# Kernel tuning notes

Measured on AMD Instinct MI355X. Metric: run time of the kernel, lower is better.

Reference implementation:

```python
import jax, jax.numpy as jnp
import numpy as np

NUM_HEADS = 12
TEMPORAL_RES = 8


def _ln(x, g, b, eps=1e-5):
    mu = jnp.mean(x, axis=-1, keepdims=True)
    var = jnp.mean((x - mu) ** 2, axis=-1, keepdims=True)
    return (x - mu) * jax.lax.rsqrt(var + eps) * g + b


def setup_inputs() -> dict:
    key = jax.random.key(0)
    ks = jax.random.split(key, 8)
    s = 0.02
    d = 768
    inp = {
        'box_tensors': jax.random.uniform(ks[0], (16, 16, 10, 4), dtype=jnp.float32),
        'box_categories': jax.random.normal(ks[1], (16, 10, d), dtype=jnp.float32) * s,
        'w1': jax.random.normal(ks[2], (4, d // 2), dtype=jnp.float32) * s,
        'w2': jax.random.normal(ks[3], (d // 2, d), dtype=jnp.float32) * s,
        'ln1_g': jnp.ones((d,), jnp.float32),
        'ln1_b': jnp.zeros((d,), jnp.float32),
        'wqkv': jax.random.normal(ks[4], (d, 3 * d), dtype=jnp.float32) * s,
        'wo': jax.random.normal(ks[5], (d, d), dtype=jnp.float32) * s,
        'bo': jnp.zeros((d,), jnp.float32),
        'ln2_g': jnp.ones((d,), jnp.float32),
        'ln2_b': jnp.zeros((d,), jnp.float32),
        'wfc1': jax.random.normal(ks[6], (d, 4 * d), dtype=jnp.float32) * s,
        'bfc1': jnp.zeros((4 * d,), jnp.float32),
        'wfc2': jax.random.normal(ks[7], (4 * d, d), dtype=jnp.float32) * s,
        'bfc2': jnp.zeros((d,), jnp.float32),
        'H': 14,
        'W': 14,
    }
    return inp


def _forward(box_tensors, box_categories, w1, w2, ln1_g, ln1_b, wqkv, wo, bo,
             ln2_g, ln2_b, wfc1, bfc1, wfc2, bfc2, H, W):
    B, T, O, _ = box_tensors.shape
    d = box_categories.shape[-1]
    # coord -> feature MLP (no biases), then pos-emb add
    h = jax.nn.relu(box_tensors @ w1)
    x = jax.nn.relu(h @ w2)                      # [B,T,O,d]
    x = x + box_categories[None]                 # broadcast over batch
    L = T * O
    x = x.reshape(B, L, d)
    # --- self-attention block (pre-LN ViT style) ---
    hn = _ln(x, ln1_g, ln1_b)
    qkv = (hn @ wqkv).reshape(B, L, 3, NUM_HEADS, d // NUM_HEADS)
    q, k, v = qkv[:, :, 0], qkv[:, :, 1], qkv[:, :, 2]   # [B,L,h,dh]
    scale = 1.0 / jnp.sqrt(jnp.asarray(d // NUM_HEADS, x.dtype))
    att = jnp.einsum('bqhd,bkhd->bhqk', q, k) * scale
    att = jax.nn.softmax(att, axis=-1)
    o = jnp.einsum('bhqk,bkhd->bqhd', att, v).reshape(B, L, d)
    x = x + (o @ wo + bo)
    hn = _ln(x, ln2_g, ln2_b)
    x = x + (jax.nn.gelu(hn @ wfc1 + bfc1, approximate=False) @ wfc2 + bfc2)
    feats = x.reshape(B, T, O, d)
    # --- box2spatial layout scatter: sum each object's feature into grid cells inside its box ---
    x1 = jnp.minimum(box_tensors[..., 0], box_tensors[..., 2])
    x2 = jnp.maximum(box_tensors[..., 0], box_tensors[..., 2])
    y1 = jnp.minimum(box_tensors[..., 1], box_tensors[..., 3])
    y2 = jnp.maximum(box_tensors[..., 1], box_tensors[..., 3])
    cy = (jnp.arange(H, dtype=x.dtype) + 0.5) / H    # [H]
    cx = (jnp.arange(W, dtype=x.dtype) + 0.5) / W    # [W]
    in_y = (cy[None, None, None, :] >= y1[..., None]) & (cy[None, None, None, :] <= y2[..., None])  # [B,T,O,H]
    in_x = (cx[None, None, None, :] >= x1[..., None]) & (cx[None, None, None, :] <= x2[..., None])  # [B,T,O,W]
    mask = (in_y[..., :, None] & in_x[..., None, :]).astype(x.dtype)  # [B,T,O,H,W]
    grid = jnp.einsum('btohw,btod->bthwd', mask, feats)               # [B,T,H,W,d]
    # temporal avg pooling to TEMPORAL_RES frames
    Tr = T // TEMPORAL_RES
    if Tr > 1:
        grid = grid.reshape(B, T // Tr, Tr, H, W, d).mean(axis=2)
    return grid.reshape(B, -1, d)                 # [B, T'*H*W, d]


def reference(box_tensors, box_categories, w1, w2, ln1_g, ln1_b, wqkv, wo, bo,
              ln2_g, ln2_b, wfc1, bfc1, wfc2, bfc2, H, W):
    return _forward(box_tensors, box_categories, w1, w2, ln1_g, ln1_b, wqkv, wo, bo,
                    ln2_g, ln2_b, wfc1, bfc1, wfc2, bfc2, H, W)
```

## Files before the change

kernel.cpp:

```cpp
#include <hip/hip_runtime.h>
#include <hip/hip_bf16.h>
#include <math.h>


#define BATCH 16
#define TT    16
#define OO    10
#define LL    160
#define BL    2560
#define DD    768
#define NH    12
#define DH    64
#define GH    14
#define GW    14
#define TGRP  8

typedef unsigned short ushort_t;
typedef __attribute__((ext_vector_type(8))) __bf16 bf16x8;
typedef __attribute__((ext_vector_type(4))) float f32x4;

__device__ __forceinline__ ushort_t f2bf(float f) {
    unsigned int u = __float_as_uint(f);
    u += 0x7fffu + ((u >> 16) & 1u);
    return (ushort_t)(u >> 16);
}

__device__ __forceinline__ int swz_xcd(int bid, int nwg) {
    return (bid & 7) * (nwg >> 3) + (bid >> 3);
}

__global__ __launch_bounds__(256)
void prep_all(const float* __restrict__ wqkv, const float* __restrict__ wo,
              const float* __restrict__ wfc1, const float* __restrict__ wfc2,
              const float* __restrict__ w2, const float* __restrict__ box,
              const float* __restrict__ w1,
              ushort_t* __restrict__ wqkvT, ushort_t* __restrict__ woT,
              ushort_t* __restrict__ wfc1T, ushort_t* __restrict__ wfc2T,
              ushort_t* __restrict__ w2T, ushort_t* __restrict__ h)
{
    __shared__ float s[32][33];
    int t = blockIdx.x;
    const float* W; ushort_t* Wt; int K, N, nx;
    if (t < 1728)      {            W = wqkv; Wt = wqkvT; K = 768;  N = 2304; nx = 72; }
    else if (t < 2304) { t -= 1728; W = wo;   Wt = woT;   K = 768;  N = 768;  nx = 24; }
    else if (t < 4608) { t -= 2304; W = wfc1; Wt = wfc1T; K = 768;  N = 3072; nx = 96; }
    else if (t < 6912) { t -= 4608; W = wfc2; Wt = wfc2T; K = 3072; N = 768;  nx = 24; }
    else if (t < 7200) { t -= 6912; W = w2;   Wt = w2T;   K = 384;  N = 768;  nx = 24; }
    else {
        const int i2 = (t - 7200) * 256 + threadIdx.x;
        const int r = i2 / 384, j = i2 - r * 384;
        const float* bx = box + (size_t)r * 4;
        float v = bx[0] * w1[j] + bx[1] * w1[384 + j] +
                  bx[2] * w1[768 + j] + bx[3] * w1[1152 + j];
        h[i2] = f2bf(fmaxf(v, 0.f));
        return;
    }
    const int n0 = (t % nx) * 32, k0 = (t / nx) * 32;
    const int tx = threadIdx.x & 31, ty = threadIdx.x >> 5;
#pragma unroll
    for (int r = 0; r < 4; ++r)
        s[ty + r * 8][tx] = W[(size_t)(k0 + ty + r * 8) * N + n0 + tx];
    __syncthreads();
#pragma unroll
    for (int r = 0; r < 4; ++r)
        Wt[(size_t)(n0 + ty + r * 8) * K + k0 + tx] = f2bf(s[tx][ty + r * 8]);
}

__global__ __launch_bounds__(256)
void ln_kernel(const float* __restrict__ in, const float* __restrict__ g,
               const float* __restrict__ bvec, ushort_t* __restrict__ out)
{
    const int r = blockIdx.x;
    const int tid = threadIdx.x;
    const float* row = in + (size_t)r * DD;
    float v0 = row[tid], v1 = row[tid + 256], v2 = row[tid + 512];
    float s  = v0 + v1 + v2;
    float s2 = v0 * v0 + v1 * v1 + v2 * v2;
#pragma unroll
    for (int off = 32; off > 0; off >>= 1) {
        s  += __shfl_down(s, off);
        s2 += __shfl_down(s2, off);
    }
    __shared__ float red[8];
    int wave = tid >> 6, lane = tid & 63;
    if (lane == 0) { red[wave] = s; red[wave + 4] = s2; }
    __syncthreads();
    s  = red[0] + red[1] + red[2] + red[3];
    s2 = red[4] + red[5] + red[6] + red[7];
    float mu  = s * (1.f / DD);
    float var = s2 * (1.f / DD) - mu * mu;
    float inv = rsqrtf(var + 1e-5f);
    ushort_t* op = out + (size_t)r * DD;
    op[tid]       = f2bf((v0 - mu) * inv * g[tid]       + bvec[tid]);
    op[tid + 256] = f2bf((v1 - mu) * inv * g[tid + 256] + bvec[tid + 256]);
    op[tid + 512] = f2bf((v2 - mu) * inv * g[tid + 512] + bvec[tid + 512]);
}

template <int MI, int NJ, int MODE, int SPLIT>
__global__ __launch_bounds__(64)
void gemm_rf2(const ushort_t* __restrict__ A, int lda,
              const ushort_t* __restrict__ Bt, int ldb,
              const float* __restrict__ bias, const float* __restrict__ cat,
              float* __restrict__ Cf, ushort_t* __restrict__ Cb,
              int ldc, int K)
{
    const int lane = threadIdx.x;
    const int l16 = lane & 15, quad = lane >> 4;

    const int nwg = gridDim.x * gridDim.y * gridDim.z;
    const int bid = blockIdx.x + gridDim.x * (blockIdx.y + gridDim.y * blockIdx.z);
    const int w   = swz_xcd(bid, nwg);
    const int bx  = w % gridDim.x;
    const int byz = w / gridDim.x;
    const int by  = byz % gridDim.y;
    const int bz  = byz / gridDim.y;

    const int row0 = by * (MI * 16), col0 = bx * (NJ * 16);
    const int Kper = K / SPLIT;
    const int k0   = bz * Kper;

    const ushort_t* ap = A  + (size_t)(row0 + l16) * lda + k0 + quad * 8;
    const ushort_t* bp = Bt + (size_t)(col0 + l16) * ldb + k0 + quad * 8;

    f32x4 acc[MI][NJ];
#pragma unroll
    for (int i = 0; i < MI; ++i)
#pragma unroll
        for (int j = 0; j < NJ; ++j) {
            acc[i][j][0] = 0.f; acc[i][j][1] = 0.f;
            acc[i][j][2] = 0.f; acc[i][j][3] = 0.f;
        }

#define LOADF2(aa, bb, kk)                                                       \
    _Pragma("unroll")                                                            \
    for (int i = 0; i < MI; ++i)                                                 \
        aa[i] = *reinterpret_cast<const bf16x8*>(ap + (size_t)(i * 16) * lda + (kk)); \
    _Pragma("unroll")                                                            \
    for (int j = 0; j < NJ; ++j)                                                 \
        bb[j] = *reinterpret_cast<const bf16x8*>(bp + (size_t)(j * 16) * ldb + (kk));
#define MFMA2(aa, bb)                                                            \
    _Pragma("unroll")                                                            \
    for (int i = 0; i < MI; ++i)                                                 \
        _Pragma("unroll")                                                        \
        for (int j = 0; j < NJ; ++j)                                             \
            acc[i][j] = __builtin_amdgcn_mfma_f32_16x16x32_bf16(aa[i], bb[j], acc[i][j], 0, 0, 0);

    bf16x8 a0[MI], b0[NJ], a1[MI], b1[NJ];
    LOADF2(a0, b0, 0)
    int kt = 0;
    for (; kt + 64 < Kper; kt += 64) {
        LOADF2(a1, b1, kt + 32)
        MFMA2(a0, b0)
        LOADF2(a0, b0, kt + 64)
        MFMA2(a1, b1)
    }
    LOADF2(a1, b1, kt + 32)
    MFMA2(a0, b0)
    MFMA2(a1, b1)
#undef LOADF2
#undef MFMA2

    const int q4 = quad * 4;
#pragma unroll
    for (int i = 0; i < MI; ++i)
#pragma unroll
        for (int j = 0; j < NJ; ++j) {
            const int gcol = col0 + j * 16 + l16;
            const float bj = (MODE == 1 || MODE == 2) ? bias[gcol] : 0.f;
#pragma unroll
            for (int r = 0; r < 4; ++r) {
                const int grow = row0 + i * 16 + q4 + r;
                const size_t idx = (size_t)grow * ldc + gcol;
                const float v = acc[i][j][r];
                if (MODE == 1) {
                    Cf[idx] += v + bj;
                } else if (MODE == 2) {
                    const float u = v + bj;
                    Cb[idx] = f2bf(0.5f * u * (1.f + erff(u * 0.70710678118654752f)));
                } else if (MODE == 3) {
                    Cb[idx] = f2bf(v);
                } else {
                    Cf[idx] = fmaxf(v, 0.f) + cat[(size_t)(grow % LL) * DD + gcol];
                }
            }
        }
}

#define GLL(gp, lp) __builtin_amdgcn_global_load_lds(                       \
    (const __attribute__((address_space(1))) void*)(gp),                     \
    (__attribute__((address_space(3))) void*)(lp), 16, 0, 0)

template <int MODE, int SPLIT>
__global__ __launch_bounds__(256)
void gemm_lds(const ushort_t* __restrict__ A, int lda,
              const ushort_t* __restrict__ Bt, int ldb,
              const float* __restrict__ bias,
              float* __restrict__ Cf, ushort_t* __restrict__ Cb,
              int ldc, int K)
{
    __shared__ ushort_t As[2][8192];
    __shared__ ushort_t Bs[2][8192];

    const int t    = threadIdx.x;
    const int wv   = t >> 6;
    const int lane = t & 63;
    const int l16  = lane & 15, quad = lane >> 4;
    const int wr   = (wv >> 1) * 64;
    const int wc   = (wv & 1) * 64;

    const int nwg = gridDim.x * gridDim.y * gridDim.z;
    const int bid = blockIdx.x + gridDim.x * (blockIdx.y + gridDim.y * blockIdx.z);
    const int w   = swz_xcd(bid, nwg);
    const int bx  = w % gridDim.x;
    const int byz = w / gridDim.x;
    const int by  = byz % gridDim.y;
    const int bz  = byz / gridDim.y;

    const int row0 = by * 128, col0 = bx * 128;
    const int Kper = K / SPLIT;
    const int k0   = bz * Kper;
    const int steps = Kper / 64;

    const ushort_t* Ag = A  + (size_t)(row0 + (t & 127)) * lda + k0 + ((t >> 7) * 8);
    const ushort_t* Bg = Bt + (size_t)(col0 + (t & 127)) * ldb + k0 + ((t >> 7) * 8);

#define STAGE(c, kk) do {                                                    \
        _Pragma("unroll")                                                    \
        for (int ii = 0; ii < 4; ++ii) {                                     \
            GLL(Ag + (kk) + ii * 16, &As[c][ii * 2048 + wv * 512]);          \
            GLL(Bg + (kk) + ii * 16, &Bs[c][ii * 2048 + wv * 512]);          \
        }                                                                    \
    } while (0)

    f32x4 acc[4][4];
#pragma unroll
    for (int i = 0; i < 4; ++i)
#pragma unroll
        for (int j = 0; j < 4; ++j) {
            acc[i][j][0] = 0.f; acc[i][j][1] = 0.f;
            acc[i][j][2] = 0.f; acc[i][j][3] = 0.f;
        }

    STAGE(0, 0);
    __syncthreads();
    int cur = 0;
    for (int s = 0; s < steps; ++s) {
        if (s + 1 < steps) STAGE(cur ^ 1, (s + 1) * 64);
#pragma unroll
        for (int ks = 0; ks < 2; ++ks) {
            bf16x8 af[4], bfr[4];
#pragma unroll
            for (int i = 0; i < 4; ++i)
                af[i] = *reinterpret_cast<const bf16x8*>(
                    &As[cur][((ks * 4 + quad) * 128 + wr + i * 16 + l16) * 8]);
#pragma unroll
            for (int j = 0; j < 4; ++j)
                bfr[j] = *reinterpret_cast<const bf16x8*>(
                    &Bs[cur][((ks * 4 + quad) * 128 + wc + j * 16 + l16) * 8]);
#pragma unroll
            for (int i = 0; i < 4; ++i)
#pragma unroll
                for (int j = 0; j < 4; ++j)
                    acc[i][j] = __builtin_amdgcn_mfma_f32_16x16x32_bf16(
                        af[i], bfr[j], acc[i][j], 0, 0, 0);
        }
        __syncthreads();
        cur ^= 1;
    }
#undef STAGE

    const int q4 = quad * 4;
    const int r0w = row0 + wr, c0w = col0 + wc;
#pragma unroll
    for (int i = 0; i < 4; ++i)
#pragma unroll
        for (int j = 0; j < 4; ++j) {
            const int gcol = c0w + j * 16 + l16;
            const float bj = (MODE == 1 || MODE == 2)
                               ? ((SPLIT == 1 || bz == 0) ? bias[gcol] : 0.f)
                               : 0.f;
#pragma unroll
            for (int r = 0; r < 4; ++r) {
                const int grow = r0w + i * 16 + q4 + r;
                const size_t idx = (size_t)grow * ldc + gcol;
                const float v = acc[i][j][r];
                if (MODE == 1) {
                    if (SPLIT > 1) atomicAdd(&Cf[idx], v + bj);
                    else           Cf[idx] += v + bj;
                } else if (MODE == 2) {
                    const float u = v + bj;
                    Cb[idx] = f2bf(0.5f * u * (1.f + erff(u * 0.70710678118654752f)));
                } else {
                    Cb[idx] = f2bf(v);
                }
            }
        }
}

#define KS_STRIDE 72
#define VT_STRIDE 168
__global__ __launch_bounds__(320)
void attention_mfma(ushort_t* __restrict__ qkv)
{
    __shared__ ushort_t Ks[160 * KS_STRIDE];
    __shared__ ushort_t Vt[64 * VT_STRIDE];
    __shared__ ushort_t Pb[5][16 * VT_STRIDE];

    const int half = blockIdx.x;
    const int b  = blockIdx.y / NH;
    const int hh = blockIdx.y % NH;
    ushort_t* basew = qkv + (size_t)b * LL * (3 * DD) + hh * DH;
    const ushort_t* base = basew;
    const int tid  = threadIdx.x;
    const int wave = tid >> 6, lane = tid & 63;
    const int l16 = lane & 15, quad = lane >> 4;

#pragma unroll
    for (int it = 0; it < 4; ++it) {
        int idx = tid + it * 320;
        int l = idx >> 3, c8 = (idx & 7) * 8;
        uint4 kv = *(const uint4*)(base + (size_t)l * (3 * DD) + DD + c8);
        *(uint4*)&Ks[l * KS_STRIDE + c8] = kv;
        uint4 vv = *(const uint4*)(base + (size_t)l * (3 * DD) + 2 * DD + c8);
        ushort_t e[8];
        *(uint4*)e = vv;
#pragma unroll
        for (int i = 0; i < 8; ++i)
            Vt[(c8 + i) * VT_STRIDE + l] = e[i];
    }

    const int q0 = half * 80 + wave * 16;
    bf16x8 qf[2];
#pragma unroll
    for (int k = 0; k < 2; ++k)
        qf[k] = *reinterpret_cast<const bf16x8*>(
            base + (size_t)(q0 + l16) * (3 * DD) + k * 32 + quad * 8);

    __syncthreads();

    f32x4 S[10];
#pragma unroll
    for (int nt = 0; nt < 10; ++nt) {
        f32x4 z = {0.f, 0.f, 0.f, 0.f};
        const ushort_t* kb = &Ks[(nt * 16 + l16) * KS_STRIDE + quad * 8];
        bf16x8 kf0 = *reinterpret_cast<const bf16x8*>(kb);
        bf16x8 kf1 = *reinterpret_cast<const bf16x8*>(kb + 32);
        f32x4 a0 = __builtin_amdgcn_mfma_f32_16x16x32_bf16(qf[0], kf0, z, 0, 0, 0);
        S[nt]    = __builtin_amdgcn_mfma_f32_16x16x32_bf16(qf[1], kf1, a0, 0, 0, 0);
    }

    {
        float mrow[4] = {-1e30f, -1e30f, -1e30f, -1e30f};
#pragma unroll
        for (int nt = 0; nt < 10; ++nt)
#pragma unroll
            for (int r = 0; r < 4; ++r) {
                S[nt][r] *= 0.125f;
                mrow[r] = fmaxf(mrow[r], S[nt][r]);
            }
#pragma unroll
        for (int r = 0; r < 4; ++r) {
            mrow[r] = fmaxf(mrow[r], __shfl_xor(mrow[r], 1));
            mrow[r] = fmaxf(mrow[r], __shfl_xor(mrow[r], 2));
            mrow[r] = fmaxf(mrow[r], __shfl_xor(mrow[r], 4));
            mrow[r] = fmaxf(mrow[r], __shfl_xor(mrow[r], 8));
        }
        float lsum[4] = {0.f, 0.f, 0.f, 0.f};
#pragma unroll
        for (int nt = 0; nt < 10; ++nt)
#pragma unroll
            for (int r = 0; r < 4; ++r) {
                float e = __expf(S[nt][r] - mrow[r]);
                S[nt][r] = e;
                lsum[r] += e;
            }
#pragma unroll
        for (int r = 0; r < 4; ++r) {
            lsum[r] += __shfl_xor(lsum[r], 1);
            lsum[r] += __shfl_xor(lsum[r], 2);
            lsum[r] += __shfl_xor(lsum[r], 4);
            lsum[r] += __shfl_xor(lsum[r], 8);
            lsum[r] = 1.f / lsum[r];
        }
#pragma unroll
        for (int nt = 0; nt < 10; ++nt)
#pragma unroll
            for (int r = 0; r < 4; ++r)
                Pb[wave][(quad * 4 + r) * VT_STRIDE + nt * 16 + l16] =
                    f2bf(S[nt][r] * lsum[r]);
    }
    asm volatile("s_waitcnt lgkmcnt(0)" ::: "memory");

#pragma unroll
    for (int dt = 0; dt < 4; ++dt) {
        f32x4 o0 = {0.f, 0.f, 0.f, 0.f};
#pragma unroll
        for (int ks = 0; ks < 5; ++ks) {
            bf16x8 vf = *reinterpret_cast<const bf16x8*>(
                &Vt[(dt * 16 + l16) * VT_STRIDE + ks * 32 + quad * 8]);
            bf16x8 p0 = *reinterpret_cast<const bf16x8*>(
                &Pb[wave][(l16) * VT_STRIDE + ks * 32 + quad * 8]);
            o0 = __builtin_amdgcn_mfma_f32_16x16x32_bf16(vf, p0, o0, 0, 0, 0);
        }
        ushort_t pk[4];
#pragma unroll
        for (int r = 0; r < 4; ++r) pk[r] = f2bf(o0[r]);
        ushort_t* dst = basew + (size_t)(q0 + l16) * (3 * DD) + dt * 16 + quad * 4;
        *(uint2*)dst = *(const uint2*)pk;
    }
}

__global__ __launch_bounds__(256)
void mask_grid(const float* __restrict__ box, const float* __restrict__ feats,
               float* __restrict__ out)
{
    const int bx2 = blockIdx.x;
    const int g = blockIdx.y;
    const int b = blockIdx.z;
    const int hh = bx2 >> 1, w0 = (bx2 & 1) * 7;
    const float cy = (hh + 0.5f) / (float)GH;
    const int tid = threadIdx.x;

    __shared__ float x1s[20], x2s[20];
    if (tid < 20) {
        int t = g * 2 + tid / OO, o = tid % OO;
        const float* bp = box + (size_t)((b * TT + t) * OO + o) * 4;
        float x1 = fminf(bp[0], bp[2]), x2 = fmaxf(bp[0], bp[2]);
        float y1 = fminf(bp[1], bp[3]), y2 = fmaxf(bp[1], bp[3]);
        bool yok = (cy >= y1) && (cy <= y2);
        x1s[tid] = yok ? x1 : 2.f;
        x2s[tid] = yok ? x2 : -2.f;
    }

    float fr[20][3];
#pragma unroll
    for (int p = 0; p < 20; ++p) {
        int r = (b * TT + g * 2 + p / OO) * OO + (p % OO);
        const float* f = feats + (size_t)r * DD;
        fr[p][0] = f[tid];
        fr[p][1] = f[tid + 256];
        fr[p][2] = f[tid + 512];
    }
    __syncthreads();

    float* obase = out + ((size_t)(b * TGRP + g) * (GH * GW) + hh * GW + w0) * DD;
    for (int w = 0; w < 7; ++w) {
        const float cx = (w0 + w + 0.5f) / (float)GW;
        float a0 = 0.f, a1 = 0.f, a2 = 0.f;
#pragma unroll
        for (int p = 0; p < 20; ++p) {
            if (cx >= x1s[p] && cx <= x2s[p]) {
                a0 += fr[p][0]; a1 += fr[p][1]; a2 += fr[p][2];
            }
        }
        float* op = obase + (size_t)w * DD;
        op[tid]       = a0 * 0.5f;
        op[tid + 256] = a1 * 0.5f;
        op[tid + 512] = a2 * 0.5f;
    }
}

extern "C" void kernel_launch(void* const* d_in, const int* in_sizes, int n_in,
                              void* d_out, int out_size, void* d_ws, size_t ws_size,
                              hipStream_t stream)
{
    const float* box  = (const float*)d_in[0];
    const float* cat  = (const float*)d_in[1];
    const float* w1   = (const float*)d_in[2];
    const float* w2   = (const float*)d_in[3];
    const float* ln1g = (const float*)d_in[4];
    const float* ln1b = (const float*)d_in[5];
    const float* wqkv = (const float*)d_in[6];
    const float* wo   = (const float*)d_in[7];
    const float* bo   = (const float*)d_in[8];
    const float* ln2g = (const float*)d_in[9];
    const float* ln2b = (const float*)d_in[10];
    const float* wfc1 = (const float*)d_in[11];
    const float* bfc1 = (const float*)d_in[12];
    const float* wfc2 = (const float*)d_in[13];
    const float* bfc2 = (const float*)d_in[14];
    float* out = (float*)d_out;

    char* wsb = (char*)d_ws;
    float*    x     = (float*)   (wsb + 0);
    ushort_t* qkvb  = (ushort_t*)(wsb + 7864320);
    ushort_t* fc1b  = qkvb;
    ushort_t* wfc2T = (ushort_t*)(wsb + 23592960);
    ushort_t* hnb   = (ushort_t*)(wsb + 28311552);
    ushort_t* wqkvT = (ushort_t*)(wsb + 32243712);
    ushort_t* woT   = (ushort_t*)(wsb + 35782656);
    ushort_t* wfc1T = (ushort_t*)(wsb + 36962304);
    ushort_t* w2T   = (ushort_t*)(wsb + 41680896);
    ushort_t* h     = (ushort_t*)(wsb + 42270720);

    prep_all<<<11040, 256, 0, stream>>>(wqkv, wo, wfc1, wfc2, w2, box, w1,
                                        wqkvT, woT, wfc1T, wfc2T, w2T, h);
    gemm_rf2<4, 4, 4, 1><<<dim3(12, 40, 1), 64, 0, stream>>>(
        h, 384, w2T, 384, nullptr, cat, x, nullptr, DD, 384);
    ln_kernel<<<BL, 256, 0, stream>>>(x, ln1g, ln1b, hnb);
    gemm_lds<3, 1><<<dim3(2304 / 128, 2560 / 128, 1), 256, 0, stream>>>(
        hnb, DD, wqkvT, DD, nullptr, nullptr, qkvb, 3 * DD, DD);
    attention_mfma<<<dim3(2, BATCH * NH), 320, 0, stream>>>(qkvb);
    gemm_lds<1, 2><<<dim3(768 / 128, 2560 / 128, 2), 256, 0, stream>>>(
        qkvb, 3 * DD, woT, DD, bo, x, nullptr, DD, DD);
    ln_kernel<<<BL, 256, 0, stream>>>(x, ln2g, ln2b, hnb);
    gemm_lds<2, 1><<<dim3(3072 / 128, 2560 / 128, 1), 256, 0, stream>>>(
        hnb, DD, wfc1T, DD, bfc1, nullptr, fc1b, 4 * DD, DD);
    gemm_lds<1, 4><<<dim3(768 / 128, 2560 / 128, 4), 256, 0, stream>>>(
        fc1b, 4 * DD, wfc2T, 4 * DD, bfc2, x, nullptr, DD, 4 * DD);
    mask_grid<<<dim3(28, TGRP, BATCH), 256, 0, stream>>>(box, x, out);
}
```

Before: 325.8 us.

## Replace LDS GEMM with triple-buffered 128x64 tile pipeline using explicit vmcnt waits

Replaces the double-buffered 128x128x64 GEMM with a 128x64 tile and K-step 32. It uses a three-stage LDS ring with explicit s_waitcnt vmcnt and raw s_barrier, so two global-to-LDS loads stay in flight while MFMAs run. Smaller tiles double the workgroup count for better CU occupancy on the modest-sized GEMMs and cut the LDS footprint. In exchange, each workgroup gets less data reuse per load, issues more barriers per K, and runs fewer MFMAs per step.

```diff
diff --git a/kernel.cpp b/kernel.cpp
--- a/kernel.cpp
+++ b/kernel.cpp
@@ -189,24 +189,24 @@
 #define GLL(gp, lp) __builtin_amdgcn_global_load_lds(                       \
     (const __attribute__((address_space(1))) void*)(gp),                     \
     (__attribute__((address_space(3))) void*)(lp), 16, 0, 0)
+#define WAITV(n) asm volatile("s_waitcnt vmcnt(" #n ")" ::: "memory")
 
 template <int MODE, int SPLIT>
 __global__ __launch_bounds__(256)
-void gemm_lds(const ushort_t* __restrict__ A, int lda,
-              const ushort_t* __restrict__ Bt, int ldb,
-              const float* __restrict__ bias,
-              float* __restrict__ Cf, ushort_t* __restrict__ Cb,
-              int ldc, int K)
-{
-    __shared__ ushort_t As[2][8192];
-    __shared__ ushort_t Bs[2][8192];
+void gemm_p3(const ushort_t* __restrict__ A, int lda,
+             const ushort_t* __restrict__ Bt, int ldb,
+             const float* __restrict__ bias,
+             float* __restrict__ Cf, ushort_t* __restrict__ Cb,
+             int ldc, int K)
+{
+    __shared__ ushort_t As[3][4096];
+    __shared__ ushort_t Bs[3][2048];
 
     const int t    = threadIdx.x;
     const int wv   = t >> 6;
     const int lane = t & 63;
     const int l16  = lane & 15, quad = lane >> 4;
-    const int wr   = (wv >> 1) * 64;
-    const int wc   = (wv & 1) * 64;
+    const int wr   = wv * 32;
 
     const int nwg = gridDim.x * gridDim.y * gridDim.z;
     const int bid = blockIdx.x + gridDim.x * (blockIdx.y + gridDim.y * blockIdx.z);
@@ -216,66 +216,67 @@
     const int by  = byz % gridDim.y;
     const int bz  = byz / gridDim.y;
 
-    const int row0 = by * 128, col0 = bx * 128;
+    const int row0 = by * 128, col0 = bx * 64;
     const int Kper = K / SPLIT;
     const int k0   = bz * Kper;
-    const int steps = Kper / 64;
+    const int steps = Kper / 32;
 
     const ushort_t* Ag = A  + (size_t)(row0 + (t & 127)) * lda + k0 + ((t >> 7) * 8);
-    const ushort_t* Bg = Bt + (size_t)(col0 + (t & 127)) * ldb + k0 + ((t >> 7) * 8);
-
-#define STAGE(c, kk) do {                                                    \
-        _Pragma("unroll")                                                    \
-        for (int ii = 0; ii < 4; ++ii) {                                     \
-            GLL(Ag + (kk) + ii * 16, &As[c][ii * 2048 + wv * 512]);          \
-            GLL(Bg + (kk) + ii * 16, &Bs[c][ii * 2048 + wv * 512]);          \
-        }                                                                    \
+    const ushort_t* Bg = Bt + (size_t)(col0 + (t & 63))  * ldb + k0 + ((t >> 6) * 8);
+
+#define STAGE3(c, kk) do {                                                   \
+        GLL(Ag + (kk),      &As[c][wv * 512]);                               \
+        GLL(Ag + (kk) + 16, &As[c][2048 + wv * 512]);                        \
+        GLL(Bg + (kk),      &Bs[c][wv * 512]);                               \
     } while (0)
 
-    f32x4 acc[4][4];
-#pragma unroll
-    for (int i = 0; i < 4; ++i)
+    f32x4 acc[2][4];
+#pragma unroll
+    for (int i = 0; i < 2; ++i)
 #pragma unroll
         for (int j = 0; j < 4; ++j) {
             acc[i][j][0] = 0.f; acc[i][j][1] = 0.f;
             acc[i][j][2] = 0.f; acc[i][j][3] = 0.f;
         }
 
-    STAGE(0, 0);
-    __syncthreads();
-    int cur = 0;
+    STAGE3(0, 0);
+    STAGE3(1, 32);
     for (int s = 0; s < steps; ++s) {
-        if (s + 1 < steps) STAGE(cur ^ 1, (s + 1) * 64);
-#pragma unroll
-        for (int ks = 0; ks < 2; ++ks) {
-            bf16x8 af[4], bfr[4];
-#pragma unroll
-            for (int i = 0; i < 4; ++i)
-                af[i] = *reinterpret_cast<const bf16x8*>(
-                    &As[cur][((ks * 4 + quad) * 128 + wr + i * 16 + l16) * 8]);
+        if (s + 1 < steps) WAITV(3); else WAITV(0);
+        __builtin_amdgcn_s_barrier();
+        __builtin_amdgcn_sched_barrier(0);
+
+        if (s + 2 < steps) STAGE3((s + 2) % 3, (s + 2) * 32);
+
+        const int cur = s % 3;
+        bf16x8 af[2], bfr[4];
+#pragma unroll
+        for (int i = 0; i < 2; ++i)
+            af[i] = *reinterpret_cast<const bf16x8*>(
+                &As[cur][(quad * 128 + wr + i * 16 + l16) * 8]);
+#pragma unroll
+        for (int j = 0; j < 4; ++j)
+            bfr[j] = *reinterpret_cast<const bf16x8*>(
+                &Bs[cur][(quad * 64 + j * 16 + l16) * 8]);
+        asm volatile("s_waitcnt lgkmcnt(0)" ::: "memory");
+        __builtin_amdgcn_sched_barrier(0);
+
+#pragma unroll
+        for (int i = 0; i < 2; ++i)
 #pragma unroll
             for (int j = 0; j < 4; ++j)
-                bfr[j] = *reinterpret_cast<const bf16x8*>(
-                    &Bs[cur][((ks * 4 + quad) * 128 + wc + j * 16 + l16) * 8]);
-#pragma unroll
-            for (int i = 0; i < 4; ++i)
-#pragma unroll
-                for (int j = 0; j < 4; ++j)
-                    acc[i][j] = __builtin_amdgcn_mfma_f32_16x16x32_bf16(
-                        af[i], bfr[j], acc[i][j], 0, 0, 0);
-        }
-        __syncthreads();
-        cur ^= 1;
-    }
-#undef STAGE
+                acc[i][j] = __builtin_amdgcn_mfma_f32_16x16x32_bf16(
+                    af[i], bfr[j], acc[i][j], 0, 0, 0);
+    }
+#undef STAGE3
 
     const int q4 = quad * 4;
-    const int r0w = row0 + wr, c0w = col0 + wc;
-#pragma unroll
-    for (int i = 0; i < 4; ++i)
+    const int r0w = row0 + wr;
+#pragma unroll
+    for (int i = 0; i < 2; ++i)
 #pragma unroll
         for (int j = 0; j < 4; ++j) {
-            const int gcol = c0w + j * 16 + l16;
+            const int gcol = col0 + j * 16 + l16;
             const float bj = (MODE == 1 || MODE == 2)
                                ? ((SPLIT == 1 || bz == 0) ? bias[gcol] : 0.f)
                                : 0.f;
@@ -498,15 +499,15 @@
     gemm_rf2<4, 4, 4, 1><<<dim3(12, 40, 1), 64, 0, stream>>>(
         h, 384, w2T, 384, nullptr, cat, x, nullptr, DD, 384);
     ln_kernel<<<BL, 256, 0, stream>>>(x, ln1g, ln1b, hnb);
-    gemm_lds<3, 1><<<dim3(2304 / 128, 2560 / 128, 1), 256, 0, stream>>>(
+    gemm_p3<3, 1><<<dim3(2304 / 64, 2560 / 128, 1), 256, 0, stream>>>(
         hnb, DD, wqkvT, DD, nullptr, nullptr, qkvb, 3 * DD, DD);
     attention_mfma<<<dim3(2, BATCH * NH), 320, 0, stream>>>(qkvb);
-    gemm_lds<1, 2><<<dim3(768 / 128, 2560 / 128, 2), 256, 0, stream>>>(
+    gemm_p3<1, 2><<<dim3(768 / 64, 2560 / 128, 2), 256, 0, stream>>>(
         qkvb, 3 * DD, woT, DD, bo, x, nullptr, DD, DD);
     ln_kernel<<<BL, 256, 0, stream>>>(x, ln2g, ln2b, hnb);
-    gemm_lds<2, 1><<<dim3(3072 / 128, 2560 / 128, 1), 256, 0, stream>>>(
+    gemm_p3<2, 1><<<dim3(3072 / 64, 2560 / 128, 1), 256, 0, stream>>>(
         hnb, DD, wfc1T, DD, bfc1, nullptr, fc1b, 4 * DD, DD);
-    gemm_lds<1, 4><<<dim3(768 / 128, 2560 / 128, 4), 256, 0, stream>>>(
+    gemm_p3<1, 4><<<dim3(768 / 64, 2560 / 128, 4), 256, 0, stream>>>(
         fc1b, 4 * DD, wfc2T, 4 * DD, bfc2, x, nullptr, DD, 4 * DD);
     mask_grid<<<dim3(28, TGRP, BATCH), 256, 0, stream>>>(box, x, out);
 }
```

Measured after the change: 339.4 us. +4.2%, slower.

## Use register-fed split-K GEMM for residual projections with deeper K splits

Applied to the files above, without the earlier changes.

Adds a new GEMM kernel that reads operands straight from global memory into registers, with no LDS staging. Each of its 2 wavefronts computes a 64x128 tile using MFMA. The output projection and FC2 residual GEMMs now use this kernel, with split-K raised to 4 and 8 and results accumulated into x through atomic adds. This aims to raise the number of workgroups and cut LDS and barrier overhead for these small-N GEMMs. The costs are more atomic traffic, higher register pressure from the large accumulator array, and less operand reuse without shared memory.

```diff
diff --git a/kernel.cpp b/kernel.cpp
--- a/kernel.cpp
+++ b/kernel.cpp
@@ -157,8 +157,6 @@
     LOADF2(a1, b1, kt + 32)
     MFMA2(a0, b0)
     MFMA2(a1, b1)
-#undef LOADF2
-#undef MFMA2
 
     const int q4 = quad * 4;
 #pragma unroll
@@ -186,6 +184,77 @@
         }
 }
 
+template <int SPLIT>
+__global__ __launch_bounds__(128)
+void gemm_rfw(const ushort_t* __restrict__ A, int lda,
+              const ushort_t* __restrict__ Bt, int ldb,
+              const float* __restrict__ bias,
+              float* __restrict__ Cf, int ldc, int K)
+{
+    constexpr int MI = 4, NJ = 8;
+    const int tid  = threadIdx.x;
+    const int wv   = tid >> 6;
+    const int lane = tid & 63;
+    const int l16 = lane & 15, quad = lane >> 4;
+
+    const int nwg = gridDim.x * gridDim.y * gridDim.z;
+    const int bid = blockIdx.x + gridDim.x * (blockIdx.y + gridDim.y * blockIdx.z);
+    const int w   = swz_xcd(bid, nwg);
+    const int bx  = w % gridDim.x;
+    const int byz = w / gridDim.x;
+    const int by  = byz % gridDim.y;
+    const int bz  = byz / gridDim.y;
+
+    const int row0 = by * 128 + wv * 64;
+    const int col0 = bx * 128;
+    const int Kper = K / SPLIT;
+    const int k0   = bz * Kper;
+
+    const ushort_t* ap = A  + (size_t)(row0 + l16) * lda + k0 + quad * 8;
+    const ushort_t* bp = Bt + (size_t)(col0 + l16) * ldb + k0 + quad * 8;
+
+    f32x4 acc[MI][NJ];
+#pragma unroll
+    for (int i = 0; i < MI; ++i)
+#pragma unroll
+        for (int j = 0; j < NJ; ++j) {
+            acc[i][j][0] = 0.f; acc[i][j][1] = 0.f;
+            acc[i][j][2] = 0.f; acc[i][j][3] = 0.f;
+        }
+
+    bf16x8 a0[MI], b0[NJ], a1[MI], b1[NJ];
+    LOADF2(a0, b0, 0)
+    int kt = 0;
+    for (; kt + 64 < Kper; kt += 64) {
+        LOADF2(a1, b1, kt + 32)
+        MFMA2(a0, b0)
+        LOADF2(a0, b0, kt + 64)
+        MFMA2(a1, b1)
+    }
+    LOADF2(a1, b1, kt + 32)
+    MFMA2(a0, b0)
+    MFMA2(a1, b1)
+#undef LOADF2
+#undef MFMA2
+
+    const int q4 = quad * 4;
+#pragma unroll
+    for (int i = 0; i < MI; ++i)
+#pragma unroll
+        for (int j = 0; j < NJ; ++j) {
+            const int gcol = col0 + j * 16 + l16;
+            const float bj = (SPLIT == 1 || bz == 0) ? bias[gcol] : 0.f;
+#pragma unroll
+            for (int r = 0; r < 4; ++r) {
+                const int grow = row0 + i * 16 + q4 + r;
+                const size_t idx = (size_t)grow * ldc + gcol;
+                const float v = acc[i][j][r];
+                if (SPLIT > 1) atomicAdd(&Cf[idx], v + bj);
+                else           Cf[idx] += v + bj;
+            }
+        }
+}
+
 #define GLL(gp, lp) __builtin_amdgcn_global_load_lds(                       \
     (const __attribute__((address_space(1))) void*)(gp),                     \
     (__attribute__((address_space(3))) void*)(lp), 16, 0, 0)
@@ -276,18 +345,13 @@
 #pragma unroll
         for (int j = 0; j < 4; ++j) {
             const int gcol = c0w + j * 16 + l16;
-            const float bj = (MODE == 1 || MODE == 2)
-                               ? ((SPLIT == 1 || bz == 0) ? bias[gcol] : 0.f)
-                               : 0.f;
+            const float bj = (MODE == 2) ? bias[gcol] : 0.f;
 #pragma unroll
             for (int r = 0; r < 4; ++r) {
                 const int grow = r0w + i * 16 + q4 + r;
                 const size_t idx = (size_t)grow * ldc + gcol;
                 const float v = acc[i][j][r];
-                if (MODE == 1) {
-                    if (SPLIT > 1) atomicAdd(&Cf[idx], v + bj);
-                    else           Cf[idx] += v + bj;
-                } else if (MODE == 2) {
+                if (MODE == 2) {
                     const float u = v + bj;
                     Cb[idx] = f2bf(0.5f * u * (1.f + erff(u * 0.70710678118654752f)));
                 } else {
@@ -501,12 +565,12 @@
     gemm_lds<3, 1><<<dim3(2304 / 128, 2560 / 128, 1), 256, 0, stream>>>(
         hnb, DD, wqkvT, DD, nullptr, nullptr, qkvb, 3 * DD, DD);
     attention_mfma<<<dim3(2, BATCH * NH), 320, 0, stream>>>(qkvb);
-    gemm_lds<1, 2><<<dim3(768 / 128, 2560 / 128, 2), 256, 0, stream>>>(
-        qkvb, 3 * DD, woT, DD, bo, x, nullptr, DD, DD);
+    gemm_rfw<4><<<dim3(768 / 128, 2560 / 128, 4), 128, 0, stream>>>(
+        qkvb, 3 * DD, woT, DD, bo, x, DD, DD);
     ln_kernel<<<BL, 256, 0, stream>>>(x, ln2g, ln2b, hnb);
     gemm_lds<2, 1><<<dim3(3072 / 128, 2560 / 128, 1), 256, 0, stream>>>(
         hnb, DD, wfc1T, DD, bfc1, nullptr, fc1b, 4 * DD, DD);
-    gemm_lds<1, 4><<<dim3(768 / 128, 2560 / 128, 4), 256, 0, stream>>>(
-        fc1b, 4 * DD, wfc2T, 4 * DD, bfc2, x, nullptr, DD, 4 * DD);
+    gemm_rfw<8><<<dim3(768 / 128, 2560 / 128, 8), 128, 0, stream>>>(
+        fc1b, 4 * DD, wfc2T, 4 * DD, bfc2, x, DD, 4 * DD);
     mask_grid<<<dim3(28, TGRP, BATCH), 256, 0, stream>>>(box, x, out);
 }
```

After: 390.4 us. +19.8%, slower.
